# Kernel tuning notes

Measured on AMD Instinct MI355X. Metric: run time of the kernel, lower is better.

## Reference

```python
import jax, jax.numpy as jnp
import numpy as np

K = 8192      # codebook_dim
D = 256       # embedding_dim
BETA = 0.25
DECAY = 0.99
EPS = 1e-05


def setup_inputs() -> dict:
    key = jax.random.key(0)
    k1, k2, k3, k4 = jax.random.split(key, 4)
    lim = 1.0 / K
    return {
        "z": jax.random.normal(k1, (8, D, 32, 32), dtype=jnp.float32),
        "embedding": jax.random.uniform(k2, (K, D), minval=-lim, maxval=lim, dtype=jnp.float32),
        "cluster_size": jax.random.uniform(k3, (K,), dtype=jnp.float32),
        "ema_w": jax.random.uniform(k4, (K, D), minval=-lim, maxval=lim, dtype=jnp.float32),
    }


def reference(z, embedding, cluster_size, ema_w):
    # z: [B, C, H, W] -> [B, H, W, C]
    zp = jnp.transpose(z, (0, 2, 3, 1))
    zf = zp.reshape(-1, D)                                  # [N, D]
    # squared L2 distance to each code: ||z||^2 + ||e||^2 - 2 z.e
    d = (jnp.sum(zf * zf, axis=1, keepdims=True)
         + jnp.sum(embedding * embedding, axis=1)
         - 2.0 * jnp.einsum("nd,kd->nk", zf, embedding))    # [N, K]
    idx = jnp.argmin(d, axis=1)                             # [N]
    z_q = embedding[idx].reshape(zp.shape)                  # [B, H, W, C]

    # EMA update (training branch), expressed with segment sums instead of
    # materializing the one-hot [N, K] matrix.
    counts = jax.ops.segment_sum(jnp.ones_like(idx, dtype=zf.dtype), idx, num_segments=K)
    new_cs = cluster_size * DECAY + (1.0 - DECAY) * counts
    n = jnp.sum(new_cs)
    new_cs = (new_cs + EPS) / (n + K * EPS) * n
    dw = jax.ops.segment_sum(zf, idx, num_segments=K)       # encodings.T @ zf
    new_ema_w = ema_w * DECAY + (1.0 - DECAY) * dw
    new_embedding = new_ema_w / new_cs[:, None]

    sg = jax.lax.stop_gradient
    loss = jnp.mean((sg(z_q) - zp) ** 2) + BETA * jnp.mean((z_q - sg(zp)) ** 2)
    # straight-through estimator, back to NCHW
    z_q_out = jnp.transpose(zp + sg(z_q - zp), (0, 3, 1, 2))
    return z_q_out, loss, idx, new_cs, new_ema_w, new_embedding
```

## Files before the change

kernel.cpp:

```cpp
#include <hip/hip_runtime.h>

#define CHW 262144
#define HWD 1024

typedef _Float16 v8h __attribute__((ext_vector_type(8)));
typedef _Float16 v4h __attribute__((ext_vector_type(4)));
typedef float    v4f __attribute__((ext_vector_type(4)));

static const unsigned OFF_ASQ  = 0;
static const unsigned OFF_BSQ  = 8192;
static const unsigned OFF_CNT  = 16384;
static const unsigned OFF_HEAD = 24576;
static const unsigned OFF_SCAL = 32768;
static const unsigned OFF_DW   = 32776;
static const unsigned OFF_PDK  = 2129928;
static const unsigned OFF_BH   = 3178504;
static const unsigned OFF_BM   = 4227080;

#define GLL(g, l) __builtin_amdgcn_global_load_lds( \
    (const __attribute__((address_space(1))) void*)(g), \
    (__attribute__((address_space(3))) void*)(l), 16, 0, 0)

__global__ __launch_bounds__(256) void k_prep(const float* __restrict__ z, const float* __restrict__ cs,
        const float* __restrict__ emb, float* __restrict__ asq, float* __restrict__ bsq,
        _Float16* __restrict__ Bh, _Float16* __restrict__ Bm,
        _Float16* __restrict__ Ah, _Float16* __restrict__ Am,
        float* __restrict__ zf32, float* __restrict__ scal) {
    int bx = blockIdx.x;
    int t = threadIdx.x;
    if (bx < 32) {
        int n = bx * 256 + t;
        const float* p = z + (size_t)(n >> 10) * CHW + (n & 1023);
        float s = 0.f;
        #pragma unroll 8
        for (int c = 0; c < 256; ++c) { float v = p[(size_t)c << 10]; s = fmaf(v, v, s); }
        asq[n] = s;
        float cv = cs[n];
        #pragma unroll
        for (int m = 1; m < 64; m <<= 1) cv += __shfl_xor(cv, m, 64);
        if ((t & 63) == 0) atomicAdd(scal + 1, cv);
    } else if (bx < 2080) {
        int w = (bx - 32) * 4 + (t >> 6);
        int lane = t & 63;
        float4 v = *(const float4*)(emb + (size_t)w * 256 + lane * 4);
        float s = v.x * v.x;
        s = fmaf(v.y, v.y, s); s = fmaf(v.z, v.z, s); s = fmaf(v.w, v.w, s);
        #pragma unroll
        for (int m = 1; m < 64; m <<= 1) s += __shfl_xor(s, m, 64);
        if (lane == 0) bsq[w] = s;
        float e0 = v.x * 8192.0f, e1 = v.y * 8192.0f, e2 = v.z * 8192.0f, e3 = v.w * 8192.0f;
        _Float16 h0 = (_Float16)e0, h1 = (_Float16)e1, h2 = (_Float16)e2, h3 = (_Float16)e3;
        v4h hv = {h0, h1, h2, h3};
        v4h mv = {(_Float16)((e0 - (float)h0) * 2048.0f),
                  (_Float16)((e1 - (float)h1) * 2048.0f),
                  (_Float16)((e2 - (float)h2) * 2048.0f),
                  (_Float16)((e3 - (float)h3) * 2048.0f)};
        *(v4h*)(Bh + (size_t)w * 256 + lane * 4) = hv;
        *(v4h*)(Bm + (size_t)w * 256 + lane * 4) = mv;
    } else {
        __shared__ float s[64][65];
        int blk = bx - 2080;
        int hw0 = (blk & 15) * 64;
        int c0  = ((blk >> 4) & 3) * 64;
        int b   = blk >> 6;
        #pragma unroll
        for (int ii = 0; ii < 16; ++ii) {
            int e = t + ii * 256;
            int c = e >> 6, x = e & 63;
            s[c][x] = z[(size_t)b * CHW + (size_t)(c0 + c) * HWD + hw0 + x];
        }
        __syncthreads();
        int n = t & 63, cseg = (t >> 6) * 16;
        _Float16 hbuf[16], mbuf[16];
        float fbuf[16];
        #pragma unroll
        for (int j = 0; j < 16; ++j) {
            float v = s[cseg + j][n];
            _Float16 h = (_Float16)v;
            float r = v - (float)h;
            fbuf[j] = v;
            hbuf[j] = h;
            mbuf[j] = (_Float16)(r * 2048.0f);
        }
        size_t off = ((size_t)b * 1024 + hw0 + n) * 256 + c0 + cseg;
        *(v8h*)(Ah + off)     = *(v8h*)(hbuf);
        *(v8h*)(Ah + off + 8) = *(v8h*)(hbuf + 8);
        *(v8h*)(Am + off)     = *(v8h*)(mbuf);
        *(v8h*)(Am + off + 8) = *(v8h*)(mbuf + 8);
        #pragma unroll
        for (int q = 0; q < 4; ++q)
            *(float4*)(zf32 + off + q * 4) = *(float4*)(fbuf + q * 4);
    }
}

__global__ __launch_bounds__(256, 2) void k_main(
        const _Float16* __restrict__ Ah, const _Float16* __restrict__ Am,
        const _Float16* __restrict__ Bh, const _Float16* __restrict__ Bm,
        const float* __restrict__ asq, const float* __restrict__ bsq,
        unsigned* __restrict__ pdk) {
    __shared__ _Float16 lds[32768];
    const int kt = blockIdx.x, nt = blockIdx.y;
    const int n0 = nt * 128, k0 = kt * 128;
    const int t = threadIdx.x;
    const int lane = t & 63, w = t >> 6;
    const int wrow = w >> 1, wcol = w & 1;
    const int lm = lane & 15, quad = lane >> 4;

    v4f acc1[4][4], acc2[4][4];
    #pragma unroll
    for (int i = 0; i < 4; ++i)
        #pragma unroll
        for (int j = 0; j < 4; ++j) { acc1[i][j] = (v4f){0.f,0.f,0.f,0.f}; acc2[i][j] = (v4f){0.f,0.f,0.f,0.f}; }

    const int row0 = t >> 2;
    const int c40 = (t & 3) ^ ((row0 >> 1) & 3);
    const char* gA0  = (const char*)Ah + (size_t)(n0 + row0) * 512 + c40 * 16;
    const char* gAm0 = (const char*)Am + (size_t)(n0 + row0) * 512 + c40 * 16;
    const char* gB0  = (const char*)Bh + (size_t)(k0 + row0) * 512 + c40 * 16;
    const char* gBm0 = (const char*)Bm + (size_t)(k0 + row0) * 512 + c40 * 16;

    int sa[4], sb[4];
    #pragma unroll
    for (int i = 0; i < 4; ++i) {
        int mr = wrow * 64 + i * 16 + lm;
        sa[i] = mr * 32 + ((quad ^ ((mr >> 1) & 3)) * 8);
        int nr = wcol * 64 + i * 16 + lm;
        sb[i] = nr * 32 + ((quad ^ ((nr >> 1) & 3)) * 8);
    }

    auto stage = [&](int cb, int buf) {
        const size_t co = (size_t)cb * 64;
        _Float16* l0 = lds + buf * 16384 + t * 8;
        _Float16* l1 = l0 + 2048;
        GLL(gA0 + co,           l0);
        GLL(gA0 + co + 32768,   l1);
        GLL(gAm0 + co,          l0 + 4096);
        GLL(gAm0 + co + 32768,  l1 + 4096);
        GLL(gB0 + co,           l0 + 8192);
        GLL(gB0 + co + 32768,   l1 + 8192);
        GLL(gBm0 + co,          l0 + 12288);
        GLL(gBm0 + co + 32768,  l1 + 12288);
    };

    stage(0, 0);
    for (int cb = 0; cb < 8; ++cb) {
        __syncthreads();
        if (cb < 7) stage(cb + 1, (cb + 1) & 1);
        const _Float16* L = lds + (cb & 1) * 16384;

        v8h fa[4], fam[4], fb[4], fbm[4];
        #pragma unroll
        for (int i = 0; i < 4; ++i) {
            fa[i]  = *(const v8h*)(L + sa[i]);
            fam[i] = *(const v8h*)(L + 4096 + sa[i]);
            fb[i]  = *(const v8h*)(L + 8192 + sb[i]);
            fbm[i] = *(const v8h*)(L + 12288 + sb[i]);
        }
        #pragma unroll
        for (int i = 0; i < 4; ++i)
            #pragma unroll
            for (int j = 0; j < 4; ++j) {
                acc1[i][j] = __builtin_amdgcn_mfma_f32_16x16x32_f16(fa[i], fb[j], acc1[i][j], 0, 0, 0);
                acc2[i][j] = __builtin_amdgcn_mfma_f32_16x16x32_f16(fa[i], fbm[j], acc2[i][j], 0, 0, 0);
                acc2[i][j] = __builtin_amdgcn_mfma_f32_16x16x32_f16(fam[i], fb[j], acc2[i][j], 0, 0, 0);
            }
    }

    float bvv[4];
    #pragma unroll
    for (int j = 0; j < 4; ++j) bvv[j] = bsq[k0 + wcol * 64 + j * 16 + lm];
    #pragma unroll
    for (int i = 0; i < 4; ++i) {
        #pragma unroll
        for (int r = 0; r < 4; ++r) {
            int m = n0 + wrow * 64 + i * 16 + quad * 4 + r;
            float av_ = asq[m];
            unsigned best = 0xFFFFFFFFu;
            #pragma unroll
            for (int j = 0; j < 4; ++j) {
                float S = fmaf(acc2[i][j][r], 4.8828125e-4f, acc1[i][j][r]) * 1.220703125e-4f;
                float dd = (av_ + bvv[j]) - 2.0f * S;
                float gv = dd - av_;
                int mi = (int)(gv * 65536.0f) + 32768;
                int col = k0 + wcol * 64 + j * 16 + lm;
                unsigned key = ((unsigned)mi << 13) | (unsigned)col;
                best = key < best ? key : best;
            }
            #pragma unroll
            for (int xm = 1; xm < 16; xm <<= 1) {
                unsigned o = __shfl_xor(best, xm, 64);
                best = o < best ? o : best;
            }
            if (lm == 0) pdk[(size_t)m * 128 + kt * 2 + wcol] = best;
        }
    }
}

__global__ __launch_bounds__(256) void k_red(const unsigned* __restrict__ pdk,
        float* __restrict__ out_idx, int* __restrict__ cnt,
        int* __restrict__ head, int* __restrict__ nxt) {
    int n = blockIdx.x * 4 + (threadIdx.x >> 6);
    int lane = threadIdx.x & 63;
    unsigned a = pdk[(size_t)n * 128 + lane];
    unsigned b = pdk[(size_t)n * 128 + 64 + lane];
    unsigned v = a < b ? a : b;
    #pragma unroll
    for (int m = 1; m < 64; m <<= 1) {
        unsigned o = __shfl_xor(v, m, 64);
        v = o < v ? o : v;
    }
    if (lane == 0) {
        int k = (int)(v & 8191u);
        out_idx[n] = (float)k;
        atomicAdd(cnt + k, 1);
        int old = atomicExch(head + k, n + 1);
        nxt[n] = old;
    }
}

__global__ __launch_bounds__(256) void k_dw(const int* __restrict__ head, const int* __restrict__ nxt,
        const float* __restrict__ zf32, float* __restrict__ dw) {
    int kk = blockIdx.x * 4 + (threadIdx.x >> 6);
    int lane = threadIdx.x & 63;
    float4 acc = {0.f, 0.f, 0.f, 0.f};
    int cur = head[kk];
    while (cur) {
        int n = cur - 1;
        float4 v = *(const float4*)(zf32 + (size_t)n * 256 + lane * 4);
        acc.x += v.x; acc.y += v.y; acc.z += v.z; acc.w += v.w;
        cur = nxt[n];
    }
    *(float4*)(dw + (size_t)kk * 256 + lane * 4) = acc;
}

__global__ __launch_bounds__(256) void k_zq(const float* __restrict__ z, const float* __restrict__ emb,
        const float* __restrict__ out_idx, float* __restrict__ out_zq, float* __restrict__ scal) {
    int n0 = blockIdx.x * 64, c00 = blockIdx.y * 64;
    int lane = threadIdx.x & 63, g = threadIdx.x >> 6;
    int n = n0 + lane;
    int b = n >> 10, hw = n & 1023;
    int idxn = (int)out_idx[n];
    const float* zr = z + (size_t)b * CHW + hw;
    const float* er = emb + (size_t)idxn * 256;
    float* oz = out_zq + (size_t)b * CHW + hw;
    float ls = 0.f;
    #pragma unroll
    for (int q = 0; q < 4; ++q) {
        int c = c00 + g * 16 + q * 4;
        float4 e4 = *(const float4*)(er + c);
        float ev[4] = {e4.x, e4.y, e4.z, e4.w};
        #pragma unroll
        for (int r = 0; r < 4; ++r) {
            float zp = zr[(size_t)(c + r) << 10];
            float dif = ev[r] - zp;
            oz[(size_t)(c + r) << 10] = zp + dif;
            ls = fmaf(dif, dif, ls);
        }
    }
    #pragma unroll
    for (int m = 1; m < 64; m <<= 1) ls += __shfl_xor(ls, m, 64);
    __shared__ float red[4];
    if (lane == 0) red[g] = ls;
    __syncthreads();
    if (threadIdx.x == 0) atomicAdd(scal, red[0] + red[1] + red[2] + red[3]);
}

__global__ __launch_bounds__(256) void k_fin(const float* __restrict__ cs, const float* __restrict__ ema,
        const float* __restrict__ dw, const float* __restrict__ scal, const int* __restrict__ cnt,
        float* __restrict__ out_ncs, float* __restrict__ out_ema,
        float* __restrict__ out_emb, float* __restrict__ out_loss) {
    int k = blockIdx.x * 4 + (threadIdx.x >> 6);
    int lane = threadIdx.x & 63;
    const float C1 = (float)(1.0 - 0.99);
    const float KEPS = (float)(8192 * 1e-5);
    float ncs0v = cs[k] * 0.99f + C1 * (float)cnt[k];
    float nsum = 0.99f * scal[1] + C1 * 8192.0f;
    float ncs = (ncs0v + 1e-5f) / (nsum + KEPS) * nsum;
    if (lane == 0) out_ncs[k] = ncs;
    size_t base = (size_t)k * 256 + lane * 4;
    float4 e4 = *(const float4*)(ema + base);
    float4 d4 = *(const float4*)(dw + base);
    float r0 = e4.x * 0.99f + C1 * d4.x;
    float r1 = e4.y * 0.99f + C1 * d4.y;
    float r2 = e4.z * 0.99f + C1 * d4.z;
    float r3 = e4.w * 0.99f + C1 * d4.w;
    out_ema[base + 0] = r0; out_ema[base + 1] = r1; out_ema[base + 2] = r2; out_ema[base + 3] = r3;
    out_emb[base + 0] = r0 / ncs; out_emb[base + 1] = r1 / ncs;
    out_emb[base + 2] = r2 / ncs; out_emb[base + 3] = r3 / ncs;
    if (blockIdx.x == 0 && threadIdx.x == 0) {
        float m = scal[0] * (1.0f / 2097152.0f);
        out_loss[0] = m + 0.25f * m;
    }
}

extern "C" void kernel_launch(void* const* d_in, const int* in_sizes, int n_in,
                              void* d_out, int out_size, void* d_ws, size_t ws_size,
                              hipStream_t stream) {
    const float* z   = (const float*)d_in[0];
    const float* emb = (const float*)d_in[1];
    const float* cs  = (const float*)d_in[2];
    const float* ema = (const float*)d_in[3];
    float* out = (float*)d_out;
    float* wsf = (float*)d_ws;

    float* asq  = wsf + OFF_ASQ;
    float* bsq  = wsf + OFF_BSQ;
    int*   cnt  = (int*)(wsf + OFF_CNT);
    int*   head = (int*)(wsf + OFF_HEAD);
    float* scal = wsf + OFF_SCAL;
    float* dw   = wsf + OFF_DW;
    unsigned* pdk = (unsigned*)(wsf + OFF_PDK);
    _Float16* Bh = (_Float16*)(wsf + OFF_BH);
    _Float16* Bm = (_Float16*)(wsf + OFF_BM);

    float* out_zq   = out;
    float* out_loss = out + 2097152;
    float* out_idx  = out + 2097153;
    float* out_ncs  = out + 2105345;
    float* out_ema  = out + 2113537;
    float* out_emb  = out + 4210689;

    float* zf32 = out;
    _Float16* Ah = (_Float16*)(out + 2097156);
    _Float16* Am = (_Float16*)(out + 2097156 + 1048576);
    int* nxt = (int*)(out + 2105345);

    hipMemsetAsync(wsf + OFF_CNT, 0, (size_t)(OFF_SCAL + 8 - OFF_CNT) * sizeof(float), stream);

    k_prep<<<2592, 256, 0, stream>>>(z, cs, emb, asq, bsq, Bh, Bm, Ah, Am, zf32, scal);
    k_main<<<dim3(64, 64), 256, 0, stream>>>(Ah, Am, Bh, Bm, asq, bsq, pdk);
    k_red<<<2048, 256, 0, stream>>>(pdk, out_idx, cnt, head, nxt);
    k_dw<<<2048, 256, 0, stream>>>(head, nxt, zf32, dw);
    k_zq<<<dim3(128, 4), 256, 0, stream>>>(z, emb, out_idx, out_zq, scal);
    k_fin<<<2048, 256, 0, stream>>>(cs, ema, dw, scal, cnt, out_ncs, out_ema, out_emb, out_loss);
}
```

Before: 260.7 us.

## Fuse dw gather into finalize, fold memset into prep, use 512-thread GEMM blocks

Removes the separate memset and k_dw launches. Zeroing of the counters and scalars moves into extra k_prep blocks, the cluster-size sum moves into k_red, and the linked-list dw gather now runs inside k_fin, so dw is never written to or read back from memory. The distance GEMM kernel switches to 512-thread blocks, each wave owning a 32x64 sub-tile, with fewer accumulators per wave and one global-to-LDS load per operand per thread. Workspace and output buffers are reshuffled so the scratch arrays fit. The risks are lower MFMA reuse per wave and serial list walks now sitting on the critical path of the finalize kernel.

```diff
diff --git a/kernel.cpp b/kernel.cpp
--- a/kernel.cpp
+++ b/kernel.cpp
@@ -12,20 +12,19 @@
 static const unsigned OFF_CNT  = 16384;
 static const unsigned OFF_HEAD = 24576;
 static const unsigned OFF_SCAL = 32768;
-static const unsigned OFF_DW   = 32776;
-static const unsigned OFF_PDK  = 2129928;
-static const unsigned OFF_BH   = 3178504;
-static const unsigned OFF_BM   = 4227080;
+static const unsigned OFF_NXT  = 32776;
+static const unsigned OFF_ZF   = 40968;
+static const unsigned OFF_BH   = 2138120;
 
 #define GLL(g, l) __builtin_amdgcn_global_load_lds( \
     (const __attribute__((address_space(1))) void*)(g), \
     (__attribute__((address_space(3))) void*)(l), 16, 0, 0)
 
-__global__ __launch_bounds__(256) void k_prep(const float* __restrict__ z, const float* __restrict__ cs,
+__global__ __launch_bounds__(256) void k_prep(const float* __restrict__ z,
         const float* __restrict__ emb, float* __restrict__ asq, float* __restrict__ bsq,
         _Float16* __restrict__ Bh, _Float16* __restrict__ Bm,
         _Float16* __restrict__ Ah, _Float16* __restrict__ Am,
-        float* __restrict__ zf32, float* __restrict__ scal) {
+        float* __restrict__ zf32, float* __restrict__ zerobase) {
     int bx = blockIdx.x;
     int t = threadIdx.x;
     if (bx < 32) {
@@ -35,10 +34,6 @@
         #pragma unroll 8
         for (int c = 0; c < 256; ++c) { float v = p[(size_t)c << 10]; s = fmaf(v, v, s); }
         asq[n] = s;
-        float cv = cs[n];
-        #pragma unroll
-        for (int m = 1; m < 64; m <<= 1) cv += __shfl_xor(cv, m, 64);
-        if ((t & 63) == 0) atomicAdd(scal + 1, cv);
     } else if (bx < 2080) {
         int w = (bx - 32) * 4 + (t >> 6);
         int lane = t & 63;
@@ -57,7 +52,7 @@
                   (_Float16)((e3 - (float)h3) * 2048.0f)};
         *(v4h*)(Bh + (size_t)w * 256 + lane * 4) = hv;
         *(v4h*)(Bm + (size_t)w * 256 + lane * 4) = mv;
-    } else {
+    } else if (bx < 2592) {
         __shared__ float s[64][65];
         int blk = bx - 2080;
         int hw0 = (blk & 15) * 64;
@@ -90,10 +85,17 @@
         #pragma unroll
         for (int q = 0; q < 4; ++q)
             *(float4*)(zf32 + off + q * 4) = *(float4*)(fbuf + q * 4);
-    }
-}
-
-__global__ __launch_bounds__(256, 2) void k_main(
+    } else {
+        int idx = (bx - 2592) * 1024 + t * 4;
+        *(float4*)(zerobase + idx) = (float4){0.f, 0.f, 0.f, 0.f};
+        if (bx == 2607 && t == 0) {
+            *(float4*)(zerobase + 16384) = (float4){0.f, 0.f, 0.f, 0.f};
+            *(float4*)(zerobase + 16388) = (float4){0.f, 0.f, 0.f, 0.f};
+        }
+    }
+}
+
+__global__ __launch_bounds__(512, 4) void k_main(
         const _Float16* __restrict__ Ah, const _Float16* __restrict__ Am,
         const _Float16* __restrict__ Bh, const _Float16* __restrict__ Bm,
         const float* __restrict__ asq, const float* __restrict__ bsq,
@@ -106,40 +108,38 @@
     const int wrow = w >> 1, wcol = w & 1;
     const int lm = lane & 15, quad = lane >> 4;
 
-    v4f acc1[4][4], acc2[4][4];
-    #pragma unroll
-    for (int i = 0; i < 4; ++i)
+    v4f acc1[2][4], acc2[2][4];
+    #pragma unroll
+    for (int i = 0; i < 2; ++i)
         #pragma unroll
         for (int j = 0; j < 4; ++j) { acc1[i][j] = (v4f){0.f,0.f,0.f,0.f}; acc2[i][j] = (v4f){0.f,0.f,0.f,0.f}; }
 
     const int row0 = t >> 2;
     const int c40 = (t & 3) ^ ((row0 >> 1) & 3);
-    const char* gA0  = (const char*)Ah + (size_t)(n0 + row0) * 512 + c40 * 16;
-    const char* gAm0 = (const char*)Am + (size_t)(n0 + row0) * 512 + c40 * 16;
-    const char* gB0  = (const char*)Bh + (size_t)(k0 + row0) * 512 + c40 * 16;
-    const char* gBm0 = (const char*)Bm + (size_t)(k0 + row0) * 512 + c40 * 16;
-
-    int sa[4], sb[4];
-    #pragma unroll
-    for (int i = 0; i < 4; ++i) {
-        int mr = wrow * 64 + i * 16 + lm;
+    const char* gA  = (const char*)Ah + (size_t)(n0 + row0) * 512 + c40 * 16;
+    const char* gAm = (const char*)Am + (size_t)(n0 + row0) * 512 + c40 * 16;
+    const char* gB  = (const char*)Bh + (size_t)(k0 + row0) * 512 + c40 * 16;
+    const char* gBm = (const char*)Bm + (size_t)(k0 + row0) * 512 + c40 * 16;
+
+    int sa[2], sb[4];
+    #pragma unroll
+    for (int i = 0; i < 2; ++i) {
+        int mr = wrow * 32 + i * 16 + lm;
         sa[i] = mr * 32 + ((quad ^ ((mr >> 1) & 3)) * 8);
-        int nr = wcol * 64 + i * 16 + lm;
-        sb[i] = nr * 32 + ((quad ^ ((nr >> 1) & 3)) * 8);
+    }
+    #pragma unroll
+    for (int j = 0; j < 4; ++j) {
+        int nr = wcol * 64 + j * 16 + lm;
+        sb[j] = nr * 32 + ((quad ^ ((nr >> 1) & 3)) * 8);
     }
 
     auto stage = [&](int cb, int buf) {
         const size_t co = (size_t)cb * 64;
-        _Float16* l0 = lds + buf * 16384 + t * 8;
-        _Float16* l1 = l0 + 2048;
-        GLL(gA0 + co,           l0);
-        GLL(gA0 + co + 32768,   l1);
-        GLL(gAm0 + co,          l0 + 4096);
-        GLL(gAm0 + co + 32768,  l1 + 4096);
-        GLL(gB0 + co,           l0 + 8192);
-        GLL(gB0 + co + 32768,   l1 + 8192);
-        GLL(gBm0 + co,          l0 + 12288);
-        GLL(gBm0 + co + 32768,  l1 + 12288);
+        _Float16* l = lds + buf * 16384 + t * 8;
+        GLL(gA + co,  l);
+        GLL(gAm + co, l + 4096);
+        GLL(gB + co,  l + 8192);
+        GLL(gBm + co, l + 12288);
     };
 
     stage(0, 0);
@@ -148,32 +148,39 @@
         if (cb < 7) stage(cb + 1, (cb + 1) & 1);
         const _Float16* L = lds + (cb & 1) * 16384;
 
-        v8h fa[4], fam[4], fb[4], fbm[4];
-        #pragma unroll
-        for (int i = 0; i < 4; ++i) {
+        v8h fa[2], fam[2];
+        #pragma unroll
+        for (int i = 0; i < 2; ++i) {
             fa[i]  = *(const v8h*)(L + sa[i]);
             fam[i] = *(const v8h*)(L + 4096 + sa[i]);
-            fb[i]  = *(const v8h*)(L + 8192 + sb[i]);
-            fbm[i] = *(const v8h*)(L + 12288 + sb[i]);
-        }
-        #pragma unroll
-        for (int i = 0; i < 4; ++i)
+        }
+        #pragma unroll
+        for (int jh = 0; jh < 2; ++jh) {
+            v8h fb0  = *(const v8h*)(L + 8192 + sb[jh * 2]);
+            v8h fb1  = *(const v8h*)(L + 8192 + sb[jh * 2 + 1]);
+            v8h fbm0 = *(const v8h*)(L + 12288 + sb[jh * 2]);
+            v8h fbm1 = *(const v8h*)(L + 12288 + sb[jh * 2 + 1]);
             #pragma unroll
-            for (int j = 0; j < 4; ++j) {
-                acc1[i][j] = __builtin_amdgcn_mfma_f32_16x16x32_f16(fa[i], fb[j], acc1[i][j], 0, 0, 0);
-                acc2[i][j] = __builtin_amdgcn_mfma_f32_16x16x32_f16(fa[i], fbm[j], acc2[i][j], 0, 0, 0);
-                acc2[i][j] = __builtin_amdgcn_mfma_f32_16x16x32_f16(fam[i], fb[j], acc2[i][j], 0, 0, 0);
+            for (int i = 0; i < 2; ++i) {
+                int j0 = jh * 2;
+                acc1[i][j0]     = __builtin_amdgcn_mfma_f32_16x16x32_f16(fa[i],  fb0,  acc1[i][j0], 0, 0, 0);
+                acc2[i][j0]     = __builtin_amdgcn_mfma_f32_16x16x32_f16(fa[i],  fbm0, acc2[i][j0], 0, 0, 0);
+                acc2[i][j0]     = __builtin_amdgcn_mfma_f32_16x16x32_f16(fam[i], fb0,  acc2[i][j0], 0, 0, 0);
+                acc1[i][j0 + 1] = __builtin_amdgcn_mfma_f32_16x16x32_f16(fa[i],  fb1,  acc1[i][j0 + 1], 0, 0, 0);
+                acc2[i][j0 + 1] = __builtin_amdgcn_mfma_f32_16x16x32_f16(fa[i],  fbm1, acc2[i][j0 + 1], 0, 0, 0);
+                acc2[i][j0 + 1] = __builtin_amdgcn_mfma_f32_16x16x32_f16(fam[i], fb1,  acc2[i][j0 + 1], 0, 0, 0);
             }
+        }
     }
 
     float bvv[4];
     #pragma unroll
     for (int j = 0; j < 4; ++j) bvv[j] = bsq[k0 + wcol * 64 + j * 16 + lm];
     #pragma unroll
-    for (int i = 0; i < 4; ++i) {
+    for (int i = 0; i < 2; ++i) {
         #pragma unroll
         for (int r = 0; r < 4; ++r) {
-            int m = n0 + wrow * 64 + i * 16 + quad * 4 + r;
+            int m = n0 + wrow * 32 + i * 16 + quad * 4 + r;
             float av_ = asq[m];
             unsigned best = 0xFFFFFFFFu;
             #pragma unroll
@@ -197,10 +204,18 @@
 }
 
 __global__ __launch_bounds__(256) void k_red(const unsigned* __restrict__ pdk,
-        float* __restrict__ out_idx, int* __restrict__ cnt,
-        int* __restrict__ head, int* __restrict__ nxt) {
-    int n = blockIdx.x * 4 + (threadIdx.x >> 6);
-    int lane = threadIdx.x & 63;
+        const float* __restrict__ cs, float* __restrict__ out_idx, int* __restrict__ cnt,
+        int* __restrict__ head, int* __restrict__ nxt, float* __restrict__ scal) {
+    int bx = blockIdx.x;
+    int t = threadIdx.x;
+    if (bx < 32) {
+        float cv = cs[bx * 256 + t];
+        #pragma unroll
+        for (int m = 1; m < 64; m <<= 1) cv += __shfl_xor(cv, m, 64);
+        if ((t & 63) == 0) atomicAdd(scal + 1, cv);
+    }
+    int n = bx * 4 + (t >> 6);
+    int lane = t & 63;
     unsigned a = pdk[(size_t)n * 128 + lane];
     unsigned b = pdk[(size_t)n * 128 + 64 + lane];
     unsigned v = a < b ? a : b;
@@ -216,21 +231,6 @@
         int old = atomicExch(head + k, n + 1);
         nxt[n] = old;
     }
-}
-
-__global__ __launch_bounds__(256) void k_dw(const int* __restrict__ head, const int* __restrict__ nxt,
-        const float* __restrict__ zf32, float* __restrict__ dw) {
-    int kk = blockIdx.x * 4 + (threadIdx.x >> 6);
-    int lane = threadIdx.x & 63;
-    float4 acc = {0.f, 0.f, 0.f, 0.f};
-    int cur = head[kk];
-    while (cur) {
-        int n = cur - 1;
-        float4 v = *(const float4*)(zf32 + (size_t)n * 256 + lane * 4);
-        acc.x += v.x; acc.y += v.y; acc.z += v.z; acc.w += v.w;
-        cur = nxt[n];
-    }
-    *(float4*)(dw + (size_t)kk * 256 + lane * 4) = acc;
 }
 
 __global__ __launch_bounds__(256) void k_zq(const float* __restrict__ z, const float* __restrict__ emb,
@@ -266,11 +266,20 @@
 }
 
 __global__ __launch_bounds__(256) void k_fin(const float* __restrict__ cs, const float* __restrict__ ema,
-        const float* __restrict__ dw, const float* __restrict__ scal, const int* __restrict__ cnt,
+        const int* __restrict__ head, const int* __restrict__ nxt, const float* __restrict__ zf32,
+        const float* __restrict__ scal, const int* __restrict__ cnt,
         float* __restrict__ out_ncs, float* __restrict__ out_ema,
         float* __restrict__ out_emb, float* __restrict__ out_loss) {
     int k = blockIdx.x * 4 + (threadIdx.x >> 6);
     int lane = threadIdx.x & 63;
+    float4 dwv = {0.f, 0.f, 0.f, 0.f};
+    int cur = head[k];
+    while (cur) {
+        int n = cur - 1;
+        float4 v = *(const float4*)(zf32 + (size_t)n * 256 + lane * 4);
+        dwv.x += v.x; dwv.y += v.y; dwv.z += v.z; dwv.w += v.w;
+        cur = nxt[n];
+    }
     const float C1 = (float)(1.0 - 0.99);
     const float KEPS = (float)(8192 * 1e-5);
     float ncs0v = cs[k] * 0.99f + C1 * (float)cnt[k];
@@ -279,11 +288,10 @@
     if (lane == 0) out_ncs[k] = ncs;
     size_t base = (size_t)k * 256 + lane * 4;
     float4 e4 = *(const float4*)(ema + base);
-    float4 d4 = *(const float4*)(dw + base);
-    float r0 = e4.x * 0.99f + C1 * d4.x;
-    float r1 = e4.y * 0.99f + C1 * d4.y;
-    float r2 = e4.z * 0.99f + C1 * d4.z;
-    float r3 = e4.w * 0.99f + C1 * d4.w;
+    float r0 = e4.x * 0.99f + C1 * dwv.x;
+    float r1 = e4.y * 0.99f + C1 * dwv.y;
+    float r2 = e4.z * 0.99f + C1 * dwv.z;
+    float r3 = e4.w * 0.99f + C1 * dwv.w;
     out_ema[base + 0] = r0; out_ema[base + 1] = r1; out_ema[base + 2] = r2; out_ema[base + 3] = r3;
     out_emb[base + 0] = r0 / ncs; out_emb[base + 1] = r1 / ncs;
     out_emb[base + 2] = r2 / ncs; out_emb[base + 3] = r3 / ncs;
@@ -308,10 +316,9 @@
     int*   cnt  = (int*)(wsf + OFF_CNT);
     int*   head = (int*)(wsf + OFF_HEAD);
     float* scal = wsf + OFF_SCAL;
-    float* dw   = wsf + OFF_DW;
-    unsigned* pdk = (unsigned*)(wsf + OFF_PDK);
+    int*   nxt  = (int*)(wsf + OFF_NXT);
+    float* zf32 = wsf + OFF_ZF;
     _Float16* Bh = (_Float16*)(wsf + OFF_BH);
-    _Float16* Bm = (_Float16*)(wsf + OFF_BM);
 
     float* out_zq   = out;
     float* out_loss = out + 2097152;
@@ -320,17 +327,14 @@
     float* out_ema  = out + 2113537;
     float* out_emb  = out + 4210689;
 
-    float* zf32 = out;
-    _Float16* Ah = (_Float16*)(out + 2097156);
-    _Float16* Am = (_Float16*)(out + 2097156 + 1048576);
-    int* nxt = (int*)(out + 2105345);
-
-    hipMemsetAsync(wsf + OFF_CNT, 0, (size_t)(OFF_SCAL + 8 - OFF_CNT) * sizeof(float), stream);
-
-    k_prep<<<2592, 256, 0, stream>>>(z, cs, emb, asq, bsq, Bh, Bm, Ah, Am, zf32, scal);
-    k_main<<<dim3(64, 64), 256, 0, stream>>>(Ah, Am, Bh, Bm, asq, bsq, pdk);
-    k_red<<<2048, 256, 0, stream>>>(pdk, out_idx, cnt, head, nxt);
-    k_dw<<<2048, 256, 0, stream>>>(head, nxt, zf32, dw);
+    unsigned* pdk = (unsigned*)out;
+    _Float16* Ah = (_Float16*)(out + 2113540);
+    _Float16* Am = (_Float16*)(out + 2113540 + 1048576);
+    _Float16* Bm = (_Float16*)(out + 4210692);
+
+    k_prep<<<2608, 256, 0, stream>>>(z, emb, asq, bsq, Bh, Bm, Ah, Am, zf32, wsf + OFF_CNT);
+    k_main<<<dim3(64, 64), 512, 0, stream>>>(Ah, Am, Bh, Bm, asq, bsq, pdk);
+    k_red<<<2048, 256, 0, stream>>>(pdk, cs, out_idx, cnt, head, nxt, scal);
     k_zq<<<dim3(128, 4), 256, 0, stream>>>(z, emb, out_idx, out_zq, scal);
-    k_fin<<<2048, 256, 0, stream>>>(cs, ema, dw, scal, cnt, out_ncs, out_ema, out_emb, out_loss);
-}
+    k_fin<<<2048, 256, 0, stream>>>(cs, ema, head, nxt, zf32, scal, cnt, out_ncs, out_ema, out_emb, out_loss);
+}
```

After: 247.4 us. 1.05x faster.
